# Kernel tuning notes

Hardware: AMD Instinct MI355X
Metric: run time of the kernel (lower is better)

The kernel has to match this reference:

```python
import jax, jax.numpy as jnp
import numpy as np

H = 16
D_MODEL = 1024
D_K = D_MODEL // H  # 64
NEG = -1e9


def setup_inputs() -> dict:
    key = jax.random.key(0)
    ks = jax.random.split(key, 9)
    nb, nw = 4, 2048
    Q = jax.random.normal(ks[0], (nb, nw, D_MODEL), dtype=jnp.float32)
    K = jax.random.normal(ks[1], (nb, nw, D_MODEL), dtype=jnp.float32)
    V = jax.random.normal(ks[2], (nb, nw, D_MODEL), dtype=jnp.float32)
    mask = jax.random.randint(ks[3], (nb, nw, nw), 0, 2, dtype=jnp.int32)
    s = 1.0 / np.sqrt(D_MODEL)
    Wq = jax.random.normal(ks[4], (D_MODEL, D_MODEL), dtype=jnp.float32) * s
    Wk = jax.random.normal(ks[5], (D_MODEL, D_MODEL), dtype=jnp.float32) * s
    Wv = jax.random.normal(ks[6], (D_MODEL, D_MODEL), dtype=jnp.float32) * s
    Wo = jax.random.normal(ks[7], (D_MODEL, D_MODEL), dtype=jnp.float32) * s
    return {"Q": Q, "K": K, "V": V, "mask": mask,
            "Wq": Wq, "Wk": Wk, "Wv": Wv, "Wo": Wo}


def reference(Q, K, V, mask, Wq, Wk, Wv, Wo):
    nb, nw, _ = Q.shape
    scaling = jnp.asarray(np.sqrt(D_K), dtype=Q.dtype)
    # nn.Linear(bias=False): y = x @ W.T; split heads -> [nb, h, nw, d_k]
    q = (Q @ Wq.T).reshape(nb, nw, H, D_K).transpose(0, 2, 1, 3)
    k = (K @ Wk.T).reshape(nb, nw, H, D_K).transpose(0, 2, 1, 3)
    v = (V @ Wv.T).reshape(nb, nw, H, D_K).transpose(0, 2, 1, 3)
    scores = jnp.einsum('bhqd,bhkd->bhqk', q, k) / scaling
    # mask broadcast over heads (unsqueeze(1) in torch)
    scores = jnp.where(mask[:, None, :, :] == 0, jnp.asarray(NEG, scores.dtype), scores)
    probs = jax.nn.softmax(scores, axis=-1)
    # dropout is identity in eval mode
    attn = jnp.einsum('bhqk,bhkd->bhqd', probs, v)
    x = attn.transpose(0, 2, 1, 3).reshape(nb, nw, D_MODEL)
    return x @ Wo.T
```

## Files before the change

### kernel.cpp

```cpp
#include <hip/hip_runtime.h>
#include <hip/hip_bf16.h>
#include <cstdint>
#include <cmath>

#define NB 4
#define NW 2048
#define DM 1024
#define NH 16
#define DK 64

typedef __attribute__((ext_vector_type(8))) short bf16x8;
typedef __attribute__((ext_vector_type(4))) float f32x4;
union cvt8 { uint4 u; __hip_bfloat16 h[8]; };

__device__ __forceinline__ void async_ld16(const void* g, void* l) {
  __builtin_amdgcn_global_load_lds((__attribute__((address_space(1))) void*)g,
                                   (__attribute__((address_space(3))) void*)l,
                                   16, 0, 0);
}

__global__ void __launch_bounds__(256) cvt_bf16(const float* __restrict__ in,
                                                __hip_bfloat16* __restrict__ out) {
  size_t i = ((size_t)blockIdx.x * 256 + threadIdx.x) * 8;
  float4 a = *(const float4*)(in + i);
  float4 b = *(const float4*)(in + i + 4);
  cvt8 c;
#pragma unroll
  for (int t = 0; t < 4; ++t) {
    c.h[t]     = __float2bfloat16(((const float*)&a)[t]);
    c.h[4 + t] = __float2bfloat16(((const float*)&b)[t]);
  }
  *(uint4*)(out + i) = c.u;
}

__global__ void __launch_bounds__(256) mask_pack(const int* __restrict__ mask,
                                                 unsigned long long* __restrict__ bits) {
  int lane = threadIdx.x & 63;
  size_t tid = (size_t)blockIdx.x * blockDim.x + threadIdx.x;
  size_t widx = tid >> 6;
  int m = mask[widx * 64 + lane];
  unsigned long long b = __ballot(m != 0);
  if (lane == 0) bits[widx] = b;
}

__global__ void __launch_bounds__(256) gemm_bt(const __hip_bfloat16* __restrict__ A,
                                               const __hip_bfloat16* __restrict__ W,
                                               __hip_bfloat16* __restrict__ C,
                                               float alpha) {
  __shared__ __align__(16) __hip_bfloat16 sA[128 * 32];
  __shared__ __align__(16) __hip_bfloat16 sB[128 * 32];
  const int tid = threadIdx.x;
  const int lane = tid & 63;
  const int l15 = lane & 15, quad = lane >> 4;
  const int rowA = blockIdx.y * 128;
  const int colB = blockIdx.x * 128;
  const int wm = ((tid >> 6) >> 1) * 64, wn = ((tid >> 6) & 1) * 64;

  const f32x4 fz = {0.f, 0.f, 0.f, 0.f};
  f32x4 acc[4][4];
#pragma unroll
  for (int i = 0; i < 4; ++i)
#pragma unroll
    for (int j = 0; j < 4; ++j) acc[i][j] = fz;

  for (int k0 = 0; k0 < DM; k0 += 32) {
#pragma unroll
    for (int j = 0; j < 2; ++j) {
      int c = j * 256 + tid;
      int r = c >> 2, col = (c & 3) * 8;
      int ldsOff = (j * 256 + (tid & ~63)) * 16;
      async_ld16(A + (size_t)(rowA + r) * DM + k0 + col, (char*)sA + ldsOff);
      async_ld16(W + (size_t)(colB + r) * DM + k0 + col, (char*)sB + ldsOff);
    }
    __syncthreads();
    bf16x8 af[4], bfr[4];
#pragma unroll
    for (int i = 0; i < 4; ++i) {
      af[i]  = *(const bf16x8*)(sA + (wm + i * 16 + l15) * 32 + quad * 8);
      bfr[i] = *(const bf16x8*)(sB + (wn + i * 16 + l15) * 32 + quad * 8);
    }
#pragma unroll
    for (int i = 0; i < 4; ++i)
#pragma unroll
      for (int j = 0; j < 4; ++j)
        acc[i][j] = __builtin_amdgcn_mfma_f32_16x16x32_bf16(af[i], bfr[j], acc[i][j], 0, 0, 0);
    __syncthreads();
  }
#pragma unroll
  for (int i = 0; i < 4; ++i) {
    int row = rowA + wm + i * 16 + quad * 4;
#pragma unroll
    for (int j = 0; j < 4; ++j) {
      int col = colB + wn + j * 16 + l15;
#pragma unroll
      for (int r = 0; r < 4; ++r)
        C[(size_t)(row + r) * DM + col] = __float2bfloat16(acc[i][j][r] * alpha);
    }
  }
}

__global__ void __launch_bounds__(256) gemm_out(const __hip_bfloat16* __restrict__ A,
                                                const __hip_bfloat16* __restrict__ W,
                                                float* __restrict__ C) {
  __shared__ __align__(16) __hip_bfloat16 sA[128 * 32];
  __shared__ __align__(16) __hip_bfloat16 sB[128 * 32];
  const int tid = threadIdx.x;
  const int lane = tid & 63;
  const int l15 = lane & 15, quad = lane >> 4;
  const int rowA = blockIdx.y * 128;
  const int colB = blockIdx.x * 128;
  const int wm = ((tid >> 6) >> 1) * 64, wn = ((tid >> 6) & 1) * 64;

  const f32x4 fz = {0.f, 0.f, 0.f, 0.f};
  f32x4 acc[4][4];
#pragma unroll
  for (int i = 0; i < 4; ++i)
#pragma unroll
    for (int j = 0; j < 4; ++j) acc[i][j] = fz;

  for (int k0 = 0; k0 < DM; k0 += 32) {
#pragma unroll
    for (int j = 0; j < 2; ++j) {
      int c = j * 256 + tid;
      int r = c >> 2, col = (c & 3) * 8;
      int ldsOff = (j * 256 + (tid & ~63)) * 16;
      async_ld16(A + (size_t)(rowA + r) * DM + k0 + col, (char*)sA + ldsOff);
      async_ld16(W + (size_t)(colB + r) * DM + k0 + col, (char*)sB + ldsOff);
    }
    __syncthreads();
    bf16x8 af[4], bfr[4];
#pragma unroll
    for (int i = 0; i < 4; ++i) {
      af[i]  = *(const bf16x8*)(sA + (wm + i * 16 + l15) * 32 + quad * 8);
      bfr[i] = *(const bf16x8*)(sB + (wn + i * 16 + l15) * 32 + quad * 8);
    }
#pragma unroll
    for (int i = 0; i < 4; ++i)
#pragma unroll
      for (int j = 0; j < 4; ++j)
        acc[i][j] = __builtin_amdgcn_mfma_f32_16x16x32_bf16(af[i], bfr[j], acc[i][j], 0, 0, 0);
    __syncthreads();
  }
#pragma unroll
  for (int i = 0; i < 4; ++i) {
    int row = rowA + wm + i * 16 + quad * 4;
#pragma unroll
    for (int j = 0; j < 4; ++j) {
      int col = colB + wn + j * 16 + l15;
#pragma unroll
      for (int r = 0; r < 4; ++r)
        C[(size_t)(row + r) * DM + col] = acc[i][j][r];
    }
  }
}

#define LDSK 72

__global__ void __launch_bounds__(256) attn_fused(const __hip_bfloat16* __restrict__ q,
                                                  const __hip_bfloat16* __restrict__ kk,
                                                  const __hip_bfloat16* __restrict__ v,
                                                  const unsigned long long* __restrict__ mbits,
                                                  __hip_bfloat16* __restrict__ o) {
  __shared__ __align__(16) __hip_bfloat16 sK[64 * LDSK];
  __shared__ __align__(16) __hip_bfloat16 sVT[64 * LDSK];
  __shared__ __align__(16) __hip_bfloat16 sP[4][16 * LDSK];

  const int tid = threadIdx.x;
  const int wave = tid >> 6, lane = tid & 63;
  const int l15 = lane & 15, quad = lane >> 4;
  const int b = blockIdx.z, h = blockIdx.y;
  const int qbase = blockIdx.x * 64 + wave * 16;

  const __hip_bfloat16* qp = q + (size_t)(b * NW + qbase + l15) * DM + h * DK + quad * 8;
  bf16x8 aq0 = *(const bf16x8*)qp;
  bf16x8 aq1 = *(const bf16x8*)(qp + 32);

  const f32x4 fz = {0.f, 0.f, 0.f, 0.f};
  f32x4 oacc[4];
  float ls[4] = {0.f, 0.f, 0.f, 0.f};
#pragma unroll
  for (int i = 0; i < 4; ++i) oacc[i] = fz;

  for (int kt = 0; kt < NW / 64; ++kt) {
    __syncthreads();
#pragma unroll
    for (int j = 0; j < 2; ++j) {
      int c = j * 256 + tid;
      int r = c >> 3, col = (c & 7) * 8;
      *(uint4*)(sK + r * LDSK + col) =
          *(const uint4*)(kk + (size_t)(b * NW + kt * 64 + r) * DM + h * DK + col);
    }
    {
      int kp = tid & 31, d0 = (tid >> 5) * 8;
      const __hip_bfloat16* vp = v + (size_t)(b * NW + kt * 64 + 2 * kp) * DM + h * DK + d0;
      uint4 r0 = *(const uint4*)vp;
      uint4 r1 = *(const uint4*)(vp + DM);
      const unsigned short* a0 = (const unsigned short*)&r0;
      const unsigned short* a1 = (const unsigned short*)&r1;
#pragma unroll
      for (int j = 0; j < 8; ++j)
        *(unsigned int*)(sVT + (d0 + j) * LDSK + 2 * kp) =
            (unsigned int)a0[j] | ((unsigned int)a1[j] << 16);
    }
    unsigned long long mw[4];
#pragma unroll
    for (int r = 0; r < 4; ++r)
      mw[r] = mbits[(size_t)(b * NW + qbase + quad * 4 + r) * (NW / 64) + kt];
    __syncthreads();

    f32x4 S[4];
#pragma unroll
    for (int nc = 0; nc < 4; ++nc) {
      bf16x8 b0 = *(const bf16x8*)(sK + (nc * 16 + l15) * LDSK + quad * 8);
      bf16x8 b1 = *(const bf16x8*)(sK + (nc * 16 + l15) * LDSK + 32 + quad * 8);
      f32x4 t = fz;
      t = __builtin_amdgcn_mfma_f32_16x16x32_bf16(aq0, b0, t, 0, 0, 0);
      t = __builtin_amdgcn_mfma_f32_16x16x32_bf16(aq1, b1, t, 0, 0, 0);
      S[nc] = t;
    }
    unsigned long long sh[4];
#pragma unroll
    for (int r = 0; r < 4; ++r) sh[r] = mw[r] >> l15;
#pragma unroll
    for (int nc = 0; nc < 4; ++nc)
#pragma unroll
      for (int r = 0; r < 4; ++r) {
        float p = __expf(S[nc][r]);
        if (!((sh[r] >> (nc * 16)) & 1ull)) p = 0.f;
        ls[r] += p;
        sP[wave][(quad * 4 + r) * LDSK + nc * 16 + l15] = __float2bfloat16(p);
      }
    __threadfence_block();

    bf16x8 ap0 = *(const bf16x8*)(&sP[wave][l15 * LDSK + quad * 8]);
    bf16x8 ap1 = *(const bf16x8*)(&sP[wave][l15 * LDSK + 32 + quad * 8]);
#pragma unroll
    for (int nc = 0; nc < 4; ++nc) {
      bf16x8 b0 = *(const bf16x8*)(sVT + (nc * 16 + l15) * LDSK + quad * 8);
      bf16x8 b1 = *(const bf16x8*)(sVT + (nc * 16 + l15) * LDSK + 32 + quad * 8);
      oacc[nc] = __builtin_amdgcn_mfma_f32_16x16x32_bf16(ap0, b0, oacc[nc], 0, 0, 0);
      oacc[nc] = __builtin_amdgcn_mfma_f32_16x16x32_bf16(ap1, b1, oacc[nc], 0, 0, 0);
    }
  }

#pragma unroll
  for (int s = 1; s < 16; s <<= 1)
#pragma unroll
    for (int r = 0; r < 4; ++r) ls[r] += __shfl_xor(ls[r], s, 64);

  float inv[4];
#pragma unroll
  for (int r = 0; r < 4; ++r) inv[r] = 1.0f / fmaxf(ls[r], 1e-30f);
#pragma unroll
  for (int nc = 0; nc < 4; ++nc)
#pragma unroll
    for (int r = 0; r < 4; ++r)
      o[(size_t)(b * NW + qbase + quad * 4 + r) * DM + h * DK + nc * 16 + l15] =
          __float2bfloat16(oacc[nc][r] * inv[r]);
}

extern "C" void kernel_launch(void* const* d_in, const int* in_sizes, int n_in,
                              void* d_out, int out_size, void* d_ws, size_t ws_size,
                              hipStream_t stream) {
  const float* Q  = (const float*)d_in[0];
  const float* K  = (const float*)d_in[1];
  const float* V  = (const float*)d_in[2];
  const int*   Mm = (const int*)d_in[3];
  const float* Wq = (const float*)d_in[4];
  const float* Wk = (const float*)d_in[5];
  const float* Wv = (const float*)d_in[6];
  const float* Wo = (const float*)d_in[7];
  float* out = (float*)d_out;

  char* ws = (char*)d_ws;
  const size_t tb = (size_t)NB * NW * DM * sizeof(__hip_bfloat16);
  const size_t wb = (size_t)DM * DM * sizeof(__hip_bfloat16);
  __hip_bfloat16* Qb   = (__hip_bfloat16*)(ws);
  __hip_bfloat16* Kb   = (__hip_bfloat16*)(ws + tb);
  __hip_bfloat16* Vb   = (__hip_bfloat16*)(ws + 2 * tb);
  __hip_bfloat16* k_ws = (__hip_bfloat16*)(ws + 3 * tb);
  __hip_bfloat16* Wb   = (__hip_bfloat16*)(ws + 4 * tb);
  unsigned long long* mbits = (unsigned long long*)(ws + 4 * tb + wb);
  __hip_bfloat16* q_ws = (__hip_bfloat16*)d_out;
  __hip_bfloat16* v_ws = Qb;
  __hip_bfloat16* a_ws = Kb;

  const int gq = (int)((size_t)NB * NW * DM / 8 / 256);
  const int gw = (int)((size_t)DM * DM / 8 / 256);
  dim3 gg(DM / 128, NB * NW / 128);

  mask_pack<<<(size_t)NB * NW * NW / 256, 256, 0, stream>>>(Mm, mbits);
  cvt_bf16<<<gq, 256, 0, stream>>>(Q, Qb);
  cvt_bf16<<<gq, 256, 0, stream>>>(K, Kb);
  cvt_bf16<<<gq, 256, 0, stream>>>(V, Vb);

  cvt_bf16<<<gw, 256, 0, stream>>>(Wq, Wb);
  gemm_bt<<<gg, 256, 0, stream>>>(Qb, Wb, q_ws, 0.125f);
  cvt_bf16<<<gw, 256, 0, stream>>>(Wk, Wb);
  gemm_bt<<<gg, 256, 0, stream>>>(Kb, Wb, k_ws, 1.0f);
  cvt_bf16<<<gw, 256, 0, stream>>>(Wv, Wb);
  gemm_bt<<<gg, 256, 0, stream>>>(Vb, Wb, v_ws, 1.0f);

  attn_fused<<<dim3(NW / 64, NH, NB), 256, 0, stream>>>(q_ws, k_ws, v_ws, mbits, a_ws);

  cvt_bf16<<<gw, 256, 0, stream>>>(Wo, Wb);
  gemm_out<<<gg, 256, 0, stream>>>(a_ws, Wb, out);
}
```

Baseline: 499.3 us.

## Batch conversions and QKV GEMMs into single launches; emit V transposed

Merges the three activation conversions, the four weight conversions and the three projection GEMMs into one batched launch each, using a grid dimension to pick the operand. The V projection epilogue now writes V directly in a per-head transposed layout (dim-major, token-minor), so the attention kernel loads V^T tiles with plain vectorized copies instead of a shuffle-transpose into LDS. This cuts launch count, fills the GPU better with larger grids, and removes per-tile transpose work in attention. The cost is scattered 8-byte stores in the V GEMM epilogue and a reshuffled workspace that uses the output buffer for staging.

```diff
diff --git a/kernel.cpp b/kernel.cpp
--- a/kernel.cpp
+++ b/kernel.cpp
@@ -19,8 +19,38 @@
                                    16, 0, 0);
 }
 
-__global__ void __launch_bounds__(256) cvt_bf16(const float* __restrict__ in,
-                                                __hip_bfloat16* __restrict__ out) {
+__device__ __forceinline__ unsigned short bf16bits(float x) {
+  __hip_bfloat16 h = __float2bfloat16(x);
+  return *(unsigned short*)&h;
+}
+
+__global__ void __launch_bounds__(256) cvt_qkv(const float* __restrict__ Q,
+                                               const float* __restrict__ K,
+                                               const float* __restrict__ V,
+                                               __hip_bfloat16* __restrict__ Qb,
+                                               __hip_bfloat16* __restrict__ Kb,
+                                               __hip_bfloat16* __restrict__ Vb) {
+  const float* in = blockIdx.y == 0 ? Q : (blockIdx.y == 1 ? K : V);
+  __hip_bfloat16* out = blockIdx.y == 0 ? Qb : (blockIdx.y == 1 ? Kb : Vb);
+  size_t i = ((size_t)blockIdx.x * 256 + threadIdx.x) * 8;
+  float4 a = *(const float4*)(in + i);
+  float4 b = *(const float4*)(in + i + 4);
+  cvt8 c;
+#pragma unroll
+  for (int t = 0; t < 4; ++t) {
+    c.h[t]     = __float2bfloat16(((const float*)&a)[t]);
+    c.h[4 + t] = __float2bfloat16(((const float*)&b)[t]);
+  }
+  *(uint4*)(out + i) = c.u;
+}
+
+__global__ void __launch_bounds__(256) cvt_w(const float* __restrict__ W0,
+                                             const float* __restrict__ W1,
+                                             const float* __restrict__ W2,
+                                             const float* __restrict__ W3,
+                                             __hip_bfloat16* __restrict__ Wb) {
+  const float* in = blockIdx.y == 0 ? W0 : (blockIdx.y == 1 ? W1 : (blockIdx.y == 2 ? W2 : W3));
+  __hip_bfloat16* out = Wb + (size_t)blockIdx.y * DM * DM;
   size_t i = ((size_t)blockIdx.x * 256 + threadIdx.x) * 8;
   float4 a = *(const float4*)(in + i);
   float4 b = *(const float4*)(in + i + 4);
@@ -43,12 +73,18 @@
   if (lane == 0) bits[widx] = b;
 }
 
-__global__ void __launch_bounds__(256) gemm_bt(const __hip_bfloat16* __restrict__ A,
-                                               const __hip_bfloat16* __restrict__ W,
-                                               __hip_bfloat16* __restrict__ C,
-                                               float alpha) {
+__global__ void __launch_bounds__(256) gemm_qkv(const __hip_bfloat16* __restrict__ Qb,
+                                                const __hip_bfloat16* __restrict__ Kb,
+                                                const __hip_bfloat16* __restrict__ Vb,
+                                                const __hip_bfloat16* __restrict__ Wb,
+                                                __hip_bfloat16* __restrict__ q_ws,
+                                                __hip_bfloat16* __restrict__ k_ws,
+                                                __hip_bfloat16* __restrict__ vt) {
   __shared__ __align__(16) __hip_bfloat16 sA[128 * 32];
   __shared__ __align__(16) __hip_bfloat16 sB[128 * 32];
+  const int z = blockIdx.z;
+  const __hip_bfloat16* A = z == 0 ? Qb : (z == 1 ? Kb : Vb);
+  const __hip_bfloat16* W = Wb + (size_t)z * DM * DM;
   const int tid = threadIdx.x;
   const int lane = tid & 63;
   const int l15 = lane & 15, quad = lane >> 4;
@@ -86,15 +122,34 @@
         acc[i][j] = __builtin_amdgcn_mfma_f32_16x16x32_bf16(af[i], bfr[j], acc[i][j], 0, 0, 0);
     __syncthreads();
   }
-#pragma unroll
-  for (int i = 0; i < 4; ++i) {
-    int row = rowA + wm + i * 16 + quad * 4;
-#pragma unroll
-    for (int j = 0; j < 4; ++j) {
-      int col = colB + wn + j * 16 + l15;
-#pragma unroll
-      for (int r = 0; r < 4; ++r)
-        C[(size_t)(row + r) * DM + col] = __float2bfloat16(acc[i][j][r] * alpha);
+
+  if (z < 2) {
+    __hip_bfloat16* C = z == 0 ? q_ws : k_ws;
+    float alpha = z == 0 ? 0.125f : 1.0f;
+#pragma unroll
+    for (int i = 0; i < 4; ++i) {
+      int row = rowA + wm + i * 16 + quad * 4;
+#pragma unroll
+      for (int j = 0; j < 4; ++j) {
+        int col = colB + wn + j * 16 + l15;
+#pragma unroll
+        for (int r = 0; r < 4; ++r)
+          C[(size_t)(row + r) * DM + col] = __float2bfloat16(acc[i][j][r] * alpha);
+      }
+    }
+  } else {
+#pragma unroll
+    for (int i = 0; i < 4; ++i) {
+      int row = rowA + wm + i * 16 + quad * 4;
+      int bb = row >> 11, tok = row & 2047;
+#pragma unroll
+      for (int j = 0; j < 4; ++j) {
+        int col = colB + wn + j * 16 + l15;
+        uint2 u;
+        u.x = (unsigned int)bf16bits(acc[i][j][0]) | ((unsigned int)bf16bits(acc[i][j][1]) << 16);
+        u.y = (unsigned int)bf16bits(acc[i][j][2]) | ((unsigned int)bf16bits(acc[i][j][3]) << 16);
+        *(uint2*)(vt + ((size_t)bb * 1024 + col) * 2048 + tok) = u;
+      }
     }
   }
 }
@@ -158,7 +213,7 @@
 
 __global__ void __launch_bounds__(256) attn_fused(const __hip_bfloat16* __restrict__ q,
                                                   const __hip_bfloat16* __restrict__ kk,
-                                                  const __hip_bfloat16* __restrict__ v,
+                                                  const __hip_bfloat16* __restrict__ vt,
                                                   const unsigned long long* __restrict__ mbits,
                                                   __hip_bfloat16* __restrict__ o) {
   __shared__ __align__(16) __hip_bfloat16 sK[64 * LDSK];
@@ -175,6 +230,8 @@
   bf16x8 aq0 = *(const bf16x8*)qp;
   bf16x8 aq1 = *(const bf16x8*)(qp + 32);
 
+  const __hip_bfloat16* vbase = vt + ((size_t)b * 1024 + h * DK) * 2048;
+
   const f32x4 fz = {0.f, 0.f, 0.f, 0.f};
   f32x4 oacc[4];
   float ls[4] = {0.f, 0.f, 0.f, 0.f};
@@ -189,18 +246,8 @@
       int r = c >> 3, col = (c & 7) * 8;
       *(uint4*)(sK + r * LDSK + col) =
           *(const uint4*)(kk + (size_t)(b * NW + kt * 64 + r) * DM + h * DK + col);
-    }
-    {
-      int kp = tid & 31, d0 = (tid >> 5) * 8;
-      const __hip_bfloat16* vp = v + (size_t)(b * NW + kt * 64 + 2 * kp) * DM + h * DK + d0;
-      uint4 r0 = *(const uint4*)vp;
-      uint4 r1 = *(const uint4*)(vp + DM);
-      const unsigned short* a0 = (const unsigned short*)&r0;
-      const unsigned short* a1 = (const unsigned short*)&r1;
-#pragma unroll
-      for (int j = 0; j < 8; ++j)
-        *(unsigned int*)(sVT + (d0 + j) * LDSK + 2 * kp) =
-            (unsigned int)a0[j] | ((unsigned int)a1[j] << 16);
+      *(uint4*)(sVT + r * LDSK + col) =
+          *(const uint4*)(vbase + (size_t)r * 2048 + kt * 64 + col);
     }
     unsigned long long mw[4];
 #pragma unroll
@@ -277,32 +324,22 @@
   const size_t wb = (size_t)DM * DM * sizeof(__hip_bfloat16);
   __hip_bfloat16* Qb   = (__hip_bfloat16*)(ws);
   __hip_bfloat16* Kb   = (__hip_bfloat16*)(ws + tb);
-  __hip_bfloat16* Vb   = (__hip_bfloat16*)(ws + 2 * tb);
-  __hip_bfloat16* k_ws = (__hip_bfloat16*)(ws + 3 * tb);
+  __hip_bfloat16* k_ws = (__hip_bfloat16*)(ws + 2 * tb);
+  __hip_bfloat16* vt   = (__hip_bfloat16*)(ws + 3 * tb);
   __hip_bfloat16* Wb   = (__hip_bfloat16*)(ws + 4 * tb);
-  unsigned long long* mbits = (unsigned long long*)(ws + 4 * tb + wb);
+  unsigned long long* mbits = (unsigned long long*)(ws + 4 * tb + 4 * wb);
   __hip_bfloat16* q_ws = (__hip_bfloat16*)d_out;
-  __hip_bfloat16* v_ws = Qb;
-  __hip_bfloat16* a_ws = Kb;
+  __hip_bfloat16* Vb   = (__hip_bfloat16*)((char*)d_out + tb);
+  __hip_bfloat16* a_ws = Qb;
 
   const int gq = (int)((size_t)NB * NW * DM / 8 / 256);
   const int gw = (int)((size_t)DM * DM / 8 / 256);
-  dim3 gg(DM / 128, NB * NW / 128);
 
   mask_pack<<<(size_t)NB * NW * NW / 256, 256, 0, stream>>>(Mm, mbits);
-  cvt_bf16<<<gq, 256, 0, stream>>>(Q, Qb);
-  cvt_bf16<<<gq, 256, 0, stream>>>(K, Kb);
-  cvt_bf16<<<gq, 256, 0, stream>>>(V, Vb);
-
-  cvt_bf16<<<gw, 256, 0, stream>>>(Wq, Wb);
-  gemm_bt<<<gg, 256, 0, stream>>>(Qb, Wb, q_ws, 0.125f);
-  cvt_bf16<<<gw, 256, 0, stream>>>(Wk, Wb);
-  gemm_bt<<<gg, 256, 0, stream>>>(Kb, Wb, k_ws, 1.0f);
-  cvt_bf16<<<gw, 256, 0, stream>>>(Wv, Wb);
-  gemm_bt<<<gg, 256, 0, stream>>>(Vb, Wb, v_ws, 1.0f);
-
-  attn_fused<<<dim3(NW / 64, NH, NB), 256, 0, stream>>>(q_ws, k_ws, v_ws, mbits, a_ws);
-
-  cvt_bf16<<<gw, 256, 0, stream>>>(Wo, Wb);
-  gemm_out<<<gg, 256, 0, stream>>>(a_ws, Wb, out);
-}
+  cvt_qkv<<<dim3(gq, 3), 256, 0, stream>>>(Q, K, V, Qb, Kb, Vb);
+  cvt_w<<<dim3(gw, 4), 256, 0, stream>>>(Wq, Wk, Wv, Wo, Wb);
+  gemm_qkv<<<dim3(DM / 128, NB * NW / 128, 3), 256, 0, stream>>>(Qb, Kb, Vb, Wb,
+                                                                 q_ws, k_ws, vt);
+  attn_fused<<<dim3(NW / 64, NH, NB), 256, 0, stream>>>(q_ws, k_ws, vt, mbits, a_ws);
+  gemm_out<<<dim3(DM / 128, NB * NW / 128), 256, 0, stream>>>(a_ws, Wb + 3 * (size_t)DM * DM, out);
+}
```

Result: faster. 475.5 us (-4.8%).
